# Performance work log

Measured on AMD Instinct MI355X. Metric: run time of the kernel, lower is better.

Reference implementation:

```python
import jax, jax.numpy as jnp
import numpy as np

NQ = 10      # num_qubits
NL = 3       # num_layers
EPS = 1e-5   # BatchNorm1d eps

# PennyLane gate conventions (wire 0 = most significant bit of the state index)

def _mat_ry(t):
    c, s = jnp.cos(t / 2), jnp.sin(t / 2)
    r0 = jnp.stack([c, -s], -1)
    r1 = jnp.stack([s, c], -1)
    return jnp.stack([r0, r1], -2).astype(jnp.complex64)

def _mat_rx(t):
    c, s = jnp.cos(t / 2), jnp.sin(t / 2)
    c = c.astype(jnp.complex64)
    js = (-1j) * s.astype(jnp.complex64)
    r0 = jnp.stack([c, js], -1)
    r1 = jnp.stack([js, c], -1)
    return jnp.stack([r0, r1], -2)

def _mat_rz(t):
    em = jnp.exp(-0.5j * t.astype(jnp.complex64))
    ep = jnp.exp(0.5j * t.astype(jnp.complex64))
    z = jnp.zeros_like(em)
    r0 = jnp.stack([em, z], -1)
    r1 = jnp.stack([z, ep], -1)
    return jnp.stack([r0, r1], -2)

def _apply_1q(state, U, q):
    # state: (B, 2**NQ); U: (2,2) shared or (B,2,2) per-sample
    B = state.shape[0]
    s = state.reshape(B, 2 ** q, 2, -1)
    if U.ndim == 3:
        s = jnp.einsum('bij,bajc->baic', U, s)
    else:
        s = jnp.einsum('ij,bajc->baic', U, s)
    return s.reshape(B, -1)

def _cnot(state, c, t):
    # control c < target t: flip target bit where control bit == 1
    B = state.shape[0]
    s = state.reshape(B, 2 ** c, 2, 2 ** (t - c - 1), 2, -1)
    s = jnp.stack([s[:, :, 0], s[:, :, 1, :, ::-1, :]], axis=2)
    return s.reshape(B, -1)

def _circuit(x, params):
    # batched statevector simulation of the full circuit
    B = x.shape[0]
    state = jnp.zeros((B, 2 ** NQ), jnp.complex64).at[:, 0].set(1.0)
    for q in range(NQ):                       # RY encoding (per-sample angles)
        state = _apply_1q(state, _mat_ry(x[:, q]), q)
    for l in range(NL):
        for q in range(NQ):                   # RZ, RX, RY trainable rotations
            state = _apply_1q(state, _mat_rz(params[l, q, 0]), q)
            state = _apply_1q(state, _mat_rx(params[l, q, 1]), q)
            state = _apply_1q(state, _mat_ry(params[l, q, 2]), q)
        for i in range(NQ - 1):               # 'full' entanglement: CNOT chain
            state = _cnot(state, i, i + 1)
    probs = state.real ** 2 + state.imag ** 2
    exps = []
    for q in range(NQ):                       # <Z_q> = P(bit_q=0) - P(bit_q=1)
        p = probs.reshape(B, 2 ** q, 2, -1).sum(axis=(1, 3))
        exps.append(p[:, 0] - p[:, 1])
    return jnp.stack(exps, axis=1)            # (B, NQ)

def setup_inputs() -> dict:
    key = jax.random.key(0)
    k1, k2 = jax.random.split(key)
    x = jax.random.normal(k1, (16384, NQ), jnp.float32)
    params = jax.random.normal(k2, (NL, NQ, 3), jnp.float32)
    gamma = jnp.ones((NQ,), jnp.float32)
    beta = jnp.zeros((NQ,), jnp.float32)
    return {"x": x, "params": params, "gamma": gamma, "beta": beta}

def reference(x, params, gamma, beta):
    out = _circuit(x, params)
    # BatchNorm1d in training mode (biased batch variance)
    mean = out.mean(axis=0)
    var = ((out - mean) ** 2).mean(axis=0)
    return gamma * (out - mean) * jax.lax.rsqrt(var + EPS) + beta
```

## Files before the change

kernel.cpp:

```cpp
#include <hip/hip_runtime.h>
#include <hip/hip_fp16.h>

#define NQ 10
#define NSAMP 16384
#define BN_EPS 1e-5f
#define SGN 0x80008000u

union H2U { __half2 h; unsigned u; };
__device__ __forceinline__ __half2 u2h(unsigned u) { H2U t; t.u = u; return t.h; }
__device__ __forceinline__ unsigned h2u(__half2 h) { H2U t; t.h = h; return t.u; }
__device__ __forceinline__ __half2 hpack(float lo, float hi) {
  return __floats2half2_rn(lo, hi);
}

template<int M>
__device__ __forceinline__ unsigned shufu(unsigned v, int a30, int a28, int a20) {
  if constexpr (M == 1) {
    return (unsigned)__builtin_amdgcn_mov_dpp((int)v, 0xB1, 0xF, 0xF, true);
  } else if constexpr (M == 2) {
    return (unsigned)__builtin_amdgcn_mov_dpp((int)v, 0x4E, 0xF, 0xF, true);
  } else if constexpr (M == 3) {
    return (unsigned)__builtin_amdgcn_mov_dpp((int)v, 0x1B, 0xF, 0xF, true);
  } else if constexpr (M < 32) {
    return (unsigned)__builtin_amdgcn_ds_swizzle((int)v, (M << 10) | 0x1F);
  } else {
    const int addr = (M == 0x30) ? a30 : (M == 0x28) ? a28 : a20;
    return (unsigned)__builtin_amdgcn_ds_bpermute(addr, (int)v);
  }
}
template<int M>
__device__ __forceinline__ __half2 shufh(__half2 v, int a30, int a28, int a20) {
  return u2h(shufu<M>(h2u(v), a30, a28, a20));
}

constexpr int ML_[3][10] = {
  {0x20,0x10,0x08,0x04,0x02,0x01, 0,   0,   0,   0},
  {0x30,0x18,0x0C,0x06,0x03,0x01, 0,   0,   0,   0},
  {0x28,0x14,0x0A,0x05,0x02,0x01, 0,   0,   0,   0}};
constexpr int MR_[3][10] = {
  {0,0,0,0,0,0,   0x8,0x4,0x2,0x1},
  {0,0,0,0,0,0x8, 0xC,0x6,0x3,0x1},
  {0,0,0,0,0x8,0x4,0xA,0x5,0x2,0x1}};
constexpr int HR_[3][10] = {
  {0,0,0,0,0,0, 0x8,0x4,0x2,0x1},
  {0,0,0,0,0,0, 0x8,0xC,0xE,0xF},
  {0,0,0,0,0,0, 0x8,0x4,0xA,0x5}};
constexpr int EHL[10] = {0x20,0x30,0x18,0x0C,0x26,0x33,0x19,0x0C,0x26,0x33};

constexpr int SMASK[12] = {0x20,0x30,0x38,0x3C,0x3E,0x3F, 0x20,0x10,0x28,0x14,0x2A,0x15};
constexpr int SIX[2][10] = {{0,1,2,3,4,5,5,5,5,5}, {6,7,8,9,10,11,10,11,10,11}};

constexpr int hibit4(int m) {
  return m >= 8 ? 8 : (m >= 4 ? 4 : (m >= 2 ? 2 : (m ? 1 : 0)));
}
constexpr bool par4(int v) { return ((v >> 3 & 1) ^ (v >> 2 & 1) ^ (v >> 1 & 1) ^ (v & 1)) != 0; }

__device__ __forceinline__ void updh(__half2& ar, __half2& ai, __half2 br, __half2 bi,
                                     __half2 WR, __half2 AWI, __half2 NAWI,
                                     __half2 AVR, __half2 VI, __half2 NVI) {
  const __half2 a0r = ar, a0i = ai;
  ar = __hfma2(WR, a0r, __hfma2(AWI, a0i, __hfma2(AVR, br, __hmul2(NVI, bi))));
  ai = __hfma2(WR, a0i, __hfma2(NAWI, a0r, __hfma2(AVR, bi, __hmul2(VI, br))));
}

template<int ML, int MR, int HR>
__device__ __forceinline__ void gateh(__half2* __restrict__ Hr, __half2* __restrict__ Hi,
                                      unsigned sgnw, int a30, int a28, int a20, uint4 cp) {
  const unsigned swi = cp.y ^ sgnw;
  const unsigned svr = cp.z ^ sgnw;
  const __half2 WR  = u2h(cp.x);
  const __half2 VI  = u2h(cp.w);
  const __half2 NVI = u2h(cp.w ^ SGN);
  const __half2 WI0 = u2h(swi);
  const __half2 WI1 = u2h(swi ^ SGN);
  const __half2 VR0 = u2h(svr);
  const __half2 VR1 = u2h(svr ^ SGN);

  if constexpr (MR == 0) {
    #pragma unroll
    for (int r = 0; r < 16; ++r) {
      const __half2 br = shufh<ML>(Hr[r], a30, a28, a20);
      const __half2 bi = shufh<ML>(Hi[r], a30, a28, a20);
      const bool p = par4(r & HR);
      updh(Hr[r], Hi[r], br, bi, WR, p ? WI1 : WI0, p ? WI0 : WI1,
           p ? VR1 : VR0, VI, NVI);
    }
  } else {
    constexpr int HB = hibit4(MR);
    #pragma unroll
    for (int r = 0; r < 16; ++r) {
      if (!(r & HB)) {
        const int r2 = r ^ MR;
        __half2 b0r, b0i, b1r, b1i;
        if constexpr (ML != 0) {
          b0r = shufh<ML>(Hr[r2], a30, a28, a20); b0i = shufh<ML>(Hi[r2], a30, a28, a20);
          b1r = shufh<ML>(Hr[r],  a30, a28, a20); b1i = shufh<ML>(Hi[r],  a30, a28, a20);
        } else {
          b0r = Hr[r2]; b0i = Hi[r2]; b1r = Hr[r]; b1i = Hi[r];
        }
        const bool pa = par4(r & HR);
        updh(Hr[r], Hi[r], b0r, b0i, WR, pa ? WI1 : WI0, pa ? WI0 : WI1,
             pa ? VR1 : VR0, VI, NVI);
        const bool pb = par4(r2 & HR);
        updh(Hr[r2], Hi[r2], b1r, b1i, WR, pb ? WI1 : WI0, pb ? WI0 : WI1,
             pb ? VR1 : VR0, VI, NVI);
      }
    }
  }
}

template<int L, int Q>
__device__ __forceinline__ void rotgh(const uint4* __restrict__ cph,
                                      __half2* Hr, __half2* Hi,
                                      const unsigned* __restrict__ sgnv,
                                      int a30, int a28, int a20) {
  const uint4 cp = cph[(L - 1) * 10 + Q];
  gateh<ML_[L][Q], MR_[L][Q], HR_[L][Q]>(Hr, Hi, sgnv[SIX[L - 1][Q]], a30, a28, a20, cp);
}

__device__ __forceinline__ void enc2(const float4 g, float xq,
                                     float& ar, float& ai, float& br, float& bi) {
  const float t = xq * 0.5f;
  const float sq = __sinf(t), cq = __cosf(t);
  ar = g.x * cq - g.z * sq;
  ai = g.y * cq + g.w * sq;
  br = g.z * cq + g.x * sq;
  bi = g.w * cq - g.y * sq;
}
__device__ __forceinline__ void cmul(float& zr, float& zi,
                                     float xr, float xi, float yr, float yi) {
  zr = xr * yr - xi * yi;
  zi = xr * yi + xi * yr;
}

__device__ __forceinline__ void build_state(const float* __restrict__ xrow,
                                            const float4* __restrict__ cg,
                                            int lane, float* __restrict__ sr,
                                            float* __restrict__ si) {
  float lr, li;
  {
    float ar, ai, br, bi;
    enc2(cg[0], xrow[0], ar, ai, br, bi);
    lr = (lane & 32) ? br : ar;
    li = (lane & 32) ? bi : ai;
  }
  #pragma unroll
  for (int q = 1; q < 6; ++q) {
    float ar, ai, br, bi;
    enc2(cg[q], xrow[q], ar, ai, br, bi);
    const int bit = 1 << (5 - q);
    const float tr = (lane & bit) ? br : ar;
    const float ti = (lane & bit) ? bi : ai;
    const float nr = lr * tr - li * ti;
    const float ni = lr * ti + li * tr;
    lr = nr; li = ni;
  }
  float ar, ai, br, bi;
  float t2r[2], t2i[2], t4r[4], t4i[4], t8r[8], t8i[8];
  enc2(cg[6], xrow[6], ar, ai, br, bi);
  cmul(t2r[0], t2i[0], lr, li, ar, ai);
  cmul(t2r[1], t2i[1], lr, li, br, bi);
  enc2(cg[7], xrow[7], ar, ai, br, bi);
  #pragma unroll
  for (int j = 0; j < 2; ++j) {
    cmul(t4r[2*j+0], t4i[2*j+0], t2r[j], t2i[j], ar, ai);
    cmul(t4r[2*j+1], t4i[2*j+1], t2r[j], t2i[j], br, bi);
  }
  enc2(cg[8], xrow[8], ar, ai, br, bi);
  #pragma unroll
  for (int j = 0; j < 4; ++j) {
    cmul(t8r[2*j+0], t8i[2*j+0], t4r[j], t4i[j], ar, ai);
    cmul(t8r[2*j+1], t8i[2*j+1], t4r[j], t4i[j], br, bi);
  }
  enc2(cg[9], xrow[9], ar, ai, br, bi);
  #pragma unroll
  for (int j = 0; j < 8; ++j) {
    cmul(sr[2*j+0], si[2*j+0], t8r[j], t8i[j], ar, ai);
    cmul(sr[2*j+1], si[2*j+1], t8r[j], t8i[j], br, bi);
  }
}

__global__ void coef_kernel(const float* __restrict__ params, float* __restrict__ coef,
                            unsigned* __restrict__ cph, float* __restrict__ stats) {
  int g = threadIdx.x;
  if (g < 20) stats[g] = 0.f;
  if (g < 30) {
    float t0 = params[g * 3 + 0] * 0.5f;
    float t1 = params[g * 3 + 1] * 0.5f;
    float t2 = params[g * 3 + 2] * 0.5f;
    float sa, ca, s2, c2, s3, c3;
    __sincosf(t0, &sa, &ca);
    __sincosf(t1, &s2, &c2);
    __sincosf(t2, &s3, &c3);
    float A = c3 * c2, Bv = s3 * s2, C = s3 * c2, D = c3 * s2;
    float wr = A * ca + Bv * sa;
    float wi = Bv * ca - A * sa;
    float vr = C * ca - D * sa;
    float vi = -(C * sa + D * ca);
    coef[g * 4 + 0] = wr;
    coef[g * 4 + 1] = wi;
    coef[g * 4 + 2] = vr;
    coef[g * 4 + 3] = vi;
    if (g >= 10) {
      int gi = g - 10;
      cph[gi * 4 + 0] = h2u(hpack(wr, wr));
      cph[gi * 4 + 1] = h2u(hpack(wi, wi));
      cph[gi * 4 + 2] = h2u(hpack(vr, vr));
      cph[gi * 4 + 3] = h2u(hpack(vi, vi));
    }
  }
}

__global__ __launch_bounds__(256, 4) void circuit_kernel(const float* __restrict__ x,
                                                         const float* __restrict__ coef,
                                                         const uint4* __restrict__ cph,
                                                         float* __restrict__ out,
                                                         float* __restrict__ stats) {
  const int lane = threadIdx.x & 63;
  const int wv = threadIdx.x >> 6;
  const int wid = __builtin_amdgcn_readfirstlane(
      (int)((blockIdx.x * blockDim.x + threadIdx.x) >> 6));
  const float4* cg = (const float4*)coef;

  const int a30 = (lane ^ 0x30) << 2;
  const int a28 = (lane ^ 0x28) << 2;
  const int a20 = (lane ^ 0x20) << 2;

  unsigned sgnv[12];
  #pragma unroll
  for (int k = 0; k < 12; ++k)
    sgnv[k] = (__builtin_popcount(lane & SMASK[k]) & 1) ? 0u : SGN;

  const int sA = wid * 2, sB = wid * 2 + 1;
  float srA[16], siA[16], srB[16], siB[16];
  build_state(x + sA * NQ, cg, lane, srA, siA);
  build_state(x + sB * NQ, cg, lane, srB, siB);
  __half2 Hr[16], Hi[16];
  #pragma unroll
  for (int r = 0; r < 16; ++r) {
    Hr[r] = hpack(srA[r], srB[r]);
    Hi[r] = hpack(siA[r], siB[r]);
  }

  rotgh<1,0>(cph,Hr,Hi,sgnv,a30,a28,a20); rotgh<1,1>(cph,Hr,Hi,sgnv,a30,a28,a20);
  rotgh<1,2>(cph,Hr,Hi,sgnv,a30,a28,a20); rotgh<1,3>(cph,Hr,Hi,sgnv,a30,a28,a20);
  rotgh<1,4>(cph,Hr,Hi,sgnv,a30,a28,a20); rotgh<1,5>(cph,Hr,Hi,sgnv,a30,a28,a20);
  rotgh<1,6>(cph,Hr,Hi,sgnv,a30,a28,a20); rotgh<1,7>(cph,Hr,Hi,sgnv,a30,a28,a20);
  rotgh<1,8>(cph,Hr,Hi,sgnv,a30,a28,a20); rotgh<1,9>(cph,Hr,Hi,sgnv,a30,a28,a20);

  rotgh<2,0>(cph,Hr,Hi,sgnv,a30,a28,a20); rotgh<2,1>(cph,Hr,Hi,sgnv,a30,a28,a20);
  rotgh<2,2>(cph,Hr,Hi,sgnv,a30,a28,a20); rotgh<2,3>(cph,Hr,Hi,sgnv,a30,a28,a20);
  rotgh<2,4>(cph,Hr,Hi,sgnv,a30,a28,a20); rotgh<2,5>(cph,Hr,Hi,sgnv,a30,a28,a20);
  rotgh<2,6>(cph,Hr,Hi,sgnv,a30,a28,a20); rotgh<2,7>(cph,Hr,Hi,sgnv,a30,a28,a20);
  rotgh<2,8>(cph,Hr,Hi,sgnv,a30,a28,a20); rotgh<2,9>(cph,Hr,Hi,sgnv,a30,a28,a20);

  __half2 T = u2h(0u), S8 = T, SC = T, S6 = T, S3 = T;
  #pragma unroll
  for (int r = 0; r < 16; ++r) {
    const __half2 P = __hfma2(Hr[r], Hr[r], __hmul2(Hi[r], Hi[r]));
    T = __hadd2(T, P);
    S8 = par4(r & 0x8) ? __hsub2(S8, P) : __hadd2(S8, P);
    SC = par4(r & 0xC) ? __hsub2(SC, P) : __hadd2(SC, P);
    S6 = par4(r & 0x6) ? __hsub2(S6, P) : __hadd2(S6, P);
    S3 = par4(r & 0x3) ? __hsub2(S3, P) : __hadd2(S3, P);
  }
  const __half2 S[10] = {T, T, T, T, T, T, S8, SC, S6, S3};
  __half2 e[10];
  #pragma unroll
  for (int q = 0; q < 10; ++q) {
    const bool neg = (__builtin_popcount(lane & EHL[q]) & 1) != 0;
    e[q] = u2h(h2u(S[q]) ^ (neg ? SGN : 0u));
  }
  #pragma unroll
  for (int q = 0; q < 10; ++q) {
    e[q] = __hadd2(e[q], shufh<0x20>(e[q], a30, a28, a20));
    e[q] = __hadd2(e[q], shufh<0x10>(e[q], a30, a28, a20));
    e[q] = __hadd2(e[q], shufh<0x08>(e[q], a30, a28, a20));
    e[q] = __hadd2(e[q], shufh<0x04>(e[q], a30, a28, a20));
    e[q] = __hadd2(e[q], shufh<0x02>(e[q], a30, a28, a20));
    e[q] = __hadd2(e[q], shufh<0x01>(e[q], a30, a28, a20));
  }

  __shared__ float red[4][20];
  if (lane == 0) {
    #pragma unroll
    for (int q = 0; q < 10; ++q) {
      const float ea = __half2float(__low2half(e[q]));
      const float eb = __half2float(__high2half(e[q]));
      out[sA * NQ + q] = ea;
      out[sB * NQ + q] = eb;
      red[wv][q]      = ea + eb;
      red[wv][10 + q] = ea * ea + eb * eb;
    }
  }
  __syncthreads();
  const int tid = threadIdx.x;
  if (tid < 20) {
    float ssum = red[0][tid] + red[1][tid] + red[2][tid] + red[3][tid];
    atomicAdd(&stats[tid], ssum);
  }
}

__global__ __launch_bounds__(256) void bn_kernel(float* __restrict__ out,
                                                 const float* __restrict__ stats,
                                                 const float* __restrict__ gamma,
                                                 const float* __restrict__ beta) {
  int i = blockIdx.x * 256 + threadIdx.x;
  if (i < NSAMP * NQ) {
    int q = i % NQ;
    float mean = stats[q] * (1.f / NSAMP);
    float var = stats[10 + q] * (1.f / NSAMP) - mean * mean;
    if (var < 0.f) var = 0.f;
    float rstd = rsqrtf(var + BN_EPS);
    float v = out[i];
    out[i] = gamma[q] * (v - mean) * rstd + beta[q];
  }
}

extern "C" void kernel_launch(void* const* d_in, const int* in_sizes, int n_in,
                              void* d_out, int out_size, void* d_ws, size_t ws_size,
                              hipStream_t stream) {
  const float* x      = (const float*)d_in[0];
  const float* params = (const float*)d_in[1];
  const float* gamma  = (const float*)d_in[2];
  const float* beta   = (const float*)d_in[3];
  float* out = (float*)d_out;
  float* stats = (float*)d_ws;
  float* coef = (float*)d_ws + 32;
  unsigned* cph = (unsigned*)((float*)d_ws + 160);

  coef_kernel<<<1, 32, 0, stream>>>(params, coef, cph, stats);
  circuit_kernel<<<NSAMP / 8, 256, 0, stream>>>(x, coef, (const uint4*)cph, out, stats);
  bn_kernel<<<(NSAMP * NQ + 255) / 256, 256, 0, stream>>>(out, stats, gamma, beta);
}
```

Before: 67.22 us.

## Roll lane-crossing gates into a runtime loop and build states sequentially to cut registers

Replaces the unrolled cross-lane gates, those with no in-register partner, with a non-unrolled loop. The loop decodes each gate's lane mask, sign mask and coefficient index from packed 64-bit constants and uses ds_bpermute for every one of them. The two samples' initial states are now built one after another in a rolled loop rather than held as four float arrays at once. The precomputed per-lane sign and address registers are reduced, and the launch-bounds occupancy hint is dropped. The aim is lower register pressure and code size, at the cost of using bpermute (an LDS-path op) for shuffles that previously used cheaper DPP or swizzle, plus loop overhead.

```diff
diff --git a/kernel.cpp b/kernel.cpp
--- a/kernel.cpp
+++ b/kernel.cpp
@@ -9,12 +9,9 @@
 union H2U { __half2 h; unsigned u; };
 __device__ __forceinline__ __half2 u2h(unsigned u) { H2U t; t.u = u; return t.h; }
 __device__ __forceinline__ unsigned h2u(__half2 h) { H2U t; t.h = h; return t.u; }
-__device__ __forceinline__ __half2 hpack(float lo, float hi) {
-  return __floats2half2_rn(lo, hi);
-}
 
 template<int M>
-__device__ __forceinline__ unsigned shufu(unsigned v, int a30, int a28, int a20) {
+__device__ __forceinline__ unsigned shufu(unsigned v, int a20) {
   if constexpr (M == 1) {
     return (unsigned)__builtin_amdgcn_mov_dpp((int)v, 0xB1, 0xF, 0xF, true);
   } else if constexpr (M == 2) {
@@ -24,13 +21,12 @@
   } else if constexpr (M < 32) {
     return (unsigned)__builtin_amdgcn_ds_swizzle((int)v, (M << 10) | 0x1F);
   } else {
-    const int addr = (M == 0x30) ? a30 : (M == 0x28) ? a28 : a20;
-    return (unsigned)__builtin_amdgcn_ds_bpermute(addr, (int)v);
+    return (unsigned)__builtin_amdgcn_ds_bpermute(a20, (int)v);
   }
 }
 template<int M>
-__device__ __forceinline__ __half2 shufh(__half2 v, int a30, int a28, int a20) {
-  return u2h(shufu<M>(h2u(v), a30, a28, a20));
+__device__ __forceinline__ __half2 shufh(__half2 v, int a20) {
+  return u2h(shufu<M>(h2u(v), a20));
 }
 
 constexpr int ML_[3][10] = {
@@ -47,8 +43,16 @@
   {0,0,0,0,0,0, 0x8,0x4,0xA,0x5}};
 constexpr int EHL[10] = {0x20,0x30,0x18,0x0C,0x26,0x33,0x19,0x0C,0x26,0x33};
 
-constexpr int SMASK[12] = {0x20,0x30,0x38,0x3C,0x3E,0x3F, 0x20,0x10,0x28,0x14,0x2A,0x15};
-constexpr int SIX[2][10] = {{0,1,2,3,4,5,5,5,5,5}, {6,7,8,9,10,11,10,11,10,11}};
+constexpr unsigned long long PK6(int a0,int a1,int a2,int a3,int a4,
+                                 int a5,int a6,int a7,int a8) {
+  unsigned long long v = 0;
+  const int a[9] = {a0,a1,a2,a3,a4,a5,a6,a7,a8};
+  for (int i = 0; i < 9; ++i) v |= (unsigned long long)(unsigned)a[i] << (6 * i);
+  return v;
+}
+constexpr unsigned long long ML64 = PK6(0x30,0x18,0x0C,0x06,0x03, 0x28,0x14,0x0A,0x05);
+constexpr unsigned long long HL64 = PK6(0x20,0x30,0x38,0x3C,0x3E, 0x20,0x10,0x28,0x14);
+constexpr unsigned long long CI64 = PK6(0,1,2,3,4, 10,11,12,13);
 
 constexpr int hibit4(int m) {
   return m >= 8 ? 8 : (m >= 4 ? 4 : (m >= 2 ? 2 : (m ? 1 : 0)));
@@ -65,7 +69,7 @@
 
 template<int ML, int MR, int HR>
 __device__ __forceinline__ void gateh(__half2* __restrict__ Hr, __half2* __restrict__ Hi,
-                                      unsigned sgnw, int a30, int a28, int a20, uint4 cp) {
+                                      unsigned sgnw, int a20, uint4 cp) {
   const unsigned swi = cp.y ^ sgnw;
   const unsigned svr = cp.z ^ sgnw;
   const __half2 WR  = u2h(cp.x);
@@ -79,8 +83,8 @@
   if constexpr (MR == 0) {
     #pragma unroll
     for (int r = 0; r < 16; ++r) {
-      const __half2 br = shufh<ML>(Hr[r], a30, a28, a20);
-      const __half2 bi = shufh<ML>(Hi[r], a30, a28, a20);
+      const __half2 br = shufh<ML>(Hr[r], a20);
+      const __half2 bi = shufh<ML>(Hi[r], a20);
       const bool p = par4(r & HR);
       updh(Hr[r], Hi[r], br, bi, WR, p ? WI1 : WI0, p ? WI0 : WI1,
            p ? VR1 : VR0, VI, NVI);
@@ -93,8 +97,8 @@
         const int r2 = r ^ MR;
         __half2 b0r, b0i, b1r, b1i;
         if constexpr (ML != 0) {
-          b0r = shufh<ML>(Hr[r2], a30, a28, a20); b0i = shufh<ML>(Hi[r2], a30, a28, a20);
-          b1r = shufh<ML>(Hr[r],  a30, a28, a20); b1i = shufh<ML>(Hi[r],  a30, a28, a20);
+          b0r = shufh<ML>(Hr[r2], a20); b0i = shufh<ML>(Hi[r2], a20);
+          b1r = shufh<ML>(Hr[r],  a20); b1i = shufh<ML>(Hi[r],  a20);
         } else {
           b0r = Hr[r2]; b0i = Hi[r2]; b1r = Hr[r]; b1i = Hi[r];
         }
@@ -112,10 +116,9 @@
 template<int L, int Q>
 __device__ __forceinline__ void rotgh(const uint4* __restrict__ cph,
                                       __half2* Hr, __half2* Hi,
-                                      const unsigned* __restrict__ sgnv,
-                                      int a30, int a28, int a20) {
+                                      unsigned sgnw, int a20) {
   const uint4 cp = cph[(L - 1) * 10 + Q];
-  gateh<ML_[L][Q], MR_[L][Q], HR_[L][Q]>(Hr, Hi, sgnv[SIX[L - 1][Q]], a30, a28, a20, cp);
+  gateh<ML_[L][Q], MR_[L][Q], HR_[L][Q]>(Hr, Hi, sgnw, a20, cp);
 }
 
 __device__ __forceinline__ void enc2(const float4 g, float xq,
@@ -203,56 +206,83 @@
     coef[g * 4 + 3] = vi;
     if (g >= 10) {
       int gi = g - 10;
-      cph[gi * 4 + 0] = h2u(hpack(wr, wr));
-      cph[gi * 4 + 1] = h2u(hpack(wi, wi));
-      cph[gi * 4 + 2] = h2u(hpack(vr, vr));
-      cph[gi * 4 + 3] = h2u(hpack(vi, vi));
-    }
-  }
-}
-
-__global__ __launch_bounds__(256, 4) void circuit_kernel(const float* __restrict__ x,
-                                                         const float* __restrict__ coef,
-                                                         const uint4* __restrict__ cph,
-                                                         float* __restrict__ out,
-                                                         float* __restrict__ stats) {
+      cph[gi * 4 + 0] = h2u(__floats2half2_rn(wr, wr));
+      cph[gi * 4 + 1] = h2u(__floats2half2_rn(wi, wi));
+      cph[gi * 4 + 2] = h2u(__floats2half2_rn(vr, vr));
+      cph[gi * 4 + 3] = h2u(__floats2half2_rn(vi, vi));
+    }
+  }
+}
+
+__global__ __launch_bounds__(256) void circuit_kernel(const float* __restrict__ x,
+                                                      const float* __restrict__ coef,
+                                                      const uint4* __restrict__ cph,
+                                                      float* __restrict__ out,
+                                                      float* __restrict__ stats) {
   const int lane = threadIdx.x & 63;
   const int wv = threadIdx.x >> 6;
   const int wid = __builtin_amdgcn_readfirstlane(
       (int)((blockIdx.x * blockDim.x + threadIdx.x) >> 6));
   const float4* cg = (const float4*)coef;
-
-  const int a30 = (lane ^ 0x30) << 2;
-  const int a28 = (lane ^ 0x28) << 2;
   const int a20 = (lane ^ 0x20) << 2;
 
-  unsigned sgnv[12];
-  #pragma unroll
-  for (int k = 0; k < 12; ++k)
-    sgnv[k] = (__builtin_popcount(lane & SMASK[k]) & 1) ? 0u : SGN;
-
-  const int sA = wid * 2, sB = wid * 2 + 1;
-  float srA[16], siA[16], srB[16], siB[16];
-  build_state(x + sA * NQ, cg, lane, srA, siA);
-  build_state(x + sB * NQ, cg, lane, srB, siB);
+  const unsigned s3F = (__builtin_popcount(lane & 0x3F) & 1) ? 0u : SGN;
+  const unsigned s2A = (__builtin_popcount(lane & 0x2A) & 1) ? 0u : SGN;
+  const unsigned s15 = (__builtin_popcount(lane & 0x15) & 1) ? 0u : SGN;
+
+  const int sA = wid * 2;
   __half2 Hr[16], Hi[16];
-  #pragma unroll
-  for (int r = 0; r < 16; ++r) {
-    Hr[r] = hpack(srA[r], srB[r]);
-    Hi[r] = hpack(siA[r], siB[r]);
-  }
-
-  rotgh<1,0>(cph,Hr,Hi,sgnv,a30,a28,a20); rotgh<1,1>(cph,Hr,Hi,sgnv,a30,a28,a20);
-  rotgh<1,2>(cph,Hr,Hi,sgnv,a30,a28,a20); rotgh<1,3>(cph,Hr,Hi,sgnv,a30,a28,a20);
-  rotgh<1,4>(cph,Hr,Hi,sgnv,a30,a28,a20); rotgh<1,5>(cph,Hr,Hi,sgnv,a30,a28,a20);
-  rotgh<1,6>(cph,Hr,Hi,sgnv,a30,a28,a20); rotgh<1,7>(cph,Hr,Hi,sgnv,a30,a28,a20);
-  rotgh<1,8>(cph,Hr,Hi,sgnv,a30,a28,a20); rotgh<1,9>(cph,Hr,Hi,sgnv,a30,a28,a20);
-
-  rotgh<2,0>(cph,Hr,Hi,sgnv,a30,a28,a20); rotgh<2,1>(cph,Hr,Hi,sgnv,a30,a28,a20);
-  rotgh<2,2>(cph,Hr,Hi,sgnv,a30,a28,a20); rotgh<2,3>(cph,Hr,Hi,sgnv,a30,a28,a20);
-  rotgh<2,4>(cph,Hr,Hi,sgnv,a30,a28,a20); rotgh<2,5>(cph,Hr,Hi,sgnv,a30,a28,a20);
-  rotgh<2,6>(cph,Hr,Hi,sgnv,a30,a28,a20); rotgh<2,7>(cph,Hr,Hi,sgnv,a30,a28,a20);
-  rotgh<2,8>(cph,Hr,Hi,sgnv,a30,a28,a20); rotgh<2,9>(cph,Hr,Hi,sgnv,a30,a28,a20);
+  #pragma unroll 1
+  for (int j = 0; j < 2; ++j) {
+    float sr[16], si[16];
+    build_state(x + (sA + j) * NQ, cg, lane, sr, si);
+    #pragma unroll
+    for (int r = 0; r < 16; ++r) {
+      const unsigned pr = h2u(__floats2half2_rn(sr[r], sr[r])) & 0xFFFFu;
+      const unsigned pi = h2u(__floats2half2_rn(si[r], si[r])) & 0xFFFFu;
+      if (j == 0) { Hr[r] = u2h(pr); Hi[r] = u2h(pi); }
+      else { Hr[r] = u2h(h2u(Hr[r]) | (pr << 16)); Hi[r] = u2h(h2u(Hi[r]) | (pi << 16)); }
+    }
+  }
+
+  auto lane_loop = [&](int g0, int g1) {
+    #pragma unroll 1
+    for (int g = g0; g < g1; ++g) {
+      const unsigned ml = (unsigned)((ML64 >> (6 * g)) & 0x3F);
+      const unsigned hl = (unsigned)((HL64 >> (6 * g)) & 0x3F);
+      const int ci = (int)((CI64 >> (6 * g)) & 0x3F);
+      const uint4 cp = cph[ci];
+      const int addr = (int)((unsigned)(lane ^ (int)ml) << 2);
+      const unsigned sgnw = (__builtin_popcount(lane & hl) & 1) ? 0u : SGN;
+      const __half2 WR  = u2h(cp.x);
+      const __half2 VI  = u2h(cp.w);
+      const __half2 NVI = u2h(cp.w ^ SGN);
+      const __half2 WI  = u2h(cp.y ^ sgnw);
+      const __half2 NWI = u2h(cp.y ^ sgnw ^ SGN);
+      const __half2 VR  = u2h(cp.z ^ sgnw);
+      #pragma unroll
+      for (int r = 0; r < 16; ++r) {
+        const __half2 br = u2h((unsigned)__builtin_amdgcn_ds_bpermute(addr, (int)h2u(Hr[r])));
+        const __half2 bi = u2h((unsigned)__builtin_amdgcn_ds_bpermute(addr, (int)h2u(Hi[r])));
+        updh(Hr[r], Hi[r], br, bi, WR, WI, NWI, VR, VI, NVI);
+      }
+    }
+  };
+
+  lane_loop(0, 5);
+  rotgh<1,5>(cph, Hr, Hi, s3F, a20);
+  rotgh<1,6>(cph, Hr, Hi, s3F, a20);
+  rotgh<1,7>(cph, Hr, Hi, s3F, a20);
+  rotgh<1,8>(cph, Hr, Hi, s3F, a20);
+  rotgh<1,9>(cph, Hr, Hi, s3F, a20);
+
+  lane_loop(5, 9);
+  rotgh<2,4>(cph, Hr, Hi, s2A, a20);
+  rotgh<2,5>(cph, Hr, Hi, s15, a20);
+  rotgh<2,6>(cph, Hr, Hi, s2A, a20);
+  rotgh<2,7>(cph, Hr, Hi, s15, a20);
+  rotgh<2,8>(cph, Hr, Hi, s2A, a20);
+  rotgh<2,9>(cph, Hr, Hi, s15, a20);
 
   __half2 T = u2h(0u), S8 = T, SC = T, S6 = T, S3 = T;
   #pragma unroll
@@ -273,12 +303,12 @@
   }
   #pragma unroll
   for (int q = 0; q < 10; ++q) {
-    e[q] = __hadd2(e[q], shufh<0x20>(e[q], a30, a28, a20));
-    e[q] = __hadd2(e[q], shufh<0x10>(e[q], a30, a28, a20));
-    e[q] = __hadd2(e[q], shufh<0x08>(e[q], a30, a28, a20));
-    e[q] = __hadd2(e[q], shufh<0x04>(e[q], a30, a28, a20));
-    e[q] = __hadd2(e[q], shufh<0x02>(e[q], a30, a28, a20));
-    e[q] = __hadd2(e[q], shufh<0x01>(e[q], a30, a28, a20));
+    e[q] = __hadd2(e[q], shufh<0x20>(e[q], a20));
+    e[q] = __hadd2(e[q], shufh<0x10>(e[q], a20));
+    e[q] = __hadd2(e[q], shufh<0x08>(e[q], a20));
+    e[q] = __hadd2(e[q], shufh<0x04>(e[q], a20));
+    e[q] = __hadd2(e[q], shufh<0x02>(e[q], a20));
+    e[q] = __hadd2(e[q], shufh<0x01>(e[q], a20));
   }
 
   __shared__ float red[4][20];
@@ -287,8 +317,8 @@
     for (int q = 0; q < 10; ++q) {
       const float ea = __half2float(__low2half(e[q]));
       const float eb = __half2float(__high2half(e[q]));
-      out[sA * NQ + q] = ea;
-      out[sB * NQ + q] = eb;
+      out[sA * NQ + q]       = ea;
+      out[(sA + 1) * NQ + q] = eb;
       red[wv][q]      = ea + eb;
       red[wv][10 + q] = ea * ea + eb * eb;
     }
```

New measurement: 72.98 us. 8.6% more time.
